# Optimization experiments

Hardware: AMD Instinct MI355X
Metric: run time of the kernel (lower is better)

Reference implementation:

```python
import jax, jax.numpy as jnp
import numpy as np

N, K, D = 131072, 256, 128


def setup_inputs() -> dict:
    key = jax.random.key(0)
    k1, k2 = jax.random.split(key, 2)
    x = jax.random.normal(k1, (N, D), dtype=jnp.float32)
    mu = jax.random.normal(k2, (K, D), dtype=jnp.float32)
    prec = jnp.ones((D,), dtype=jnp.float32)
    return {"x": x, "mu": mu, "prec": prec}


def reference(x, mu, prec):
    # measure[n,k] = -0.5 * sum_d prec[d] * (x[n,d] - mu[k,d])**2
    # Expanded quadratic form avoids materializing the (N,K,D) diff tensor:
    #   sum_d prec*(x-mu)^2 = sum_d prec*x^2 - 2*sum_d (prec*x)*mu + sum_d prec*mu^2
    x_sq = jnp.einsum('nd,d->n', x * x, prec)            # (N,)
    mu_sq = jnp.einsum('kd,d->k', mu * mu, prec)         # (K,)
    cross = jnp.einsum('nd,d,kd->nk', x, prec, mu)       # (N,K)
    m = -0.5 * (x_sq[:, None] - 2.0 * cross + mu_sq[None, :])  # (N,K)
    return -jnp.sum(jax.nn.logsumexp(m, axis=1))
```

## Files before the change

kernel.cpp:

```cpp
#include <hip/hip_runtime.h>
#include <hip/hip_bf16.h>

#define N_ROWS 131072
#define K_MIX  256
#define D_DIM  128
#define LDSB_STRIDE 136
#define B_CHUNKS (K_MIX * LDSB_STRIDE / 8)

typedef float  f32x4  __attribute__((ext_vector_type(4)));
typedef short  bf16x8 __attribute__((ext_vector_type(8)));

__device__ inline bf16x8 pack8(float4 a, float4 b) {
    union { bf16x8 v; __hip_bfloat162 h[4]; } u;
    u.h[0] = __float22bfloat162_rn(make_float2(a.x, a.y));
    u.h[1] = __float22bfloat162_rn(make_float2(a.z, a.w));
    u.h[2] = __float22bfloat162_rn(make_float2(b.x, b.y));
    u.h[3] = __float22bfloat162_rn(make_float2(b.z, b.w));
    return u.v;
}

__global__ void prep_kernel(const float* __restrict__ mu,
                            const float* __restrict__ prec,
                            unsigned short* __restrict__ Bp,
                            float* __restrict__ musq)
{
    int idx = blockIdx.x * 256 + threadIdx.x;
    int row = idx >> 5;
    int c4  = idx & 31;
    float4 mv = ((const float4*)mu)[idx];
    float4 pv = ((const float4*)prec)[c4];
    float px = mv.x * pv.x, py = mv.y * pv.y, pz = mv.z * pv.z, pw = mv.w * pv.w;
    union { ushort4 u4; __hip_bfloat162 h[2]; } h;
    h.h[0] = __float22bfloat162_rn(make_float2(px, py));
    h.h[1] = __float22bfloat162_rn(make_float2(pz, pw));
    *(ushort4*)&Bp[row * LDSB_STRIDE + c4 * 4] = h.u4;
    if (c4 == 31) {
        bf16x8 z = (bf16x8)0;
        *(bf16x8*)&Bp[row * LDSB_STRIDE + 128] = z;
    }
    float ps = px * mv.x + py * mv.y + pz * mv.z + pw * mv.w;
    ps += __shfl_xor(ps, 1);  ps += __shfl_xor(ps, 2);
    ps += __shfl_xor(ps, 4);  ps += __shfl_xor(ps, 8);
    ps += __shfl_xor(ps, 16);
    if ((threadIdx.x & 31) == 0) musq[row] = 0.5f * ps;
}

__global__ __launch_bounds__(256, 2)
void mixture_main(const float* __restrict__ x,
                  const unsigned short* __restrict__ Bp,
                  const float* __restrict__ musqg,
                  const float* __restrict__ prec,
                  float* __restrict__ out)
{
    __shared__ __align__(16) unsigned short sB[K_MIX * LDSB_STRIDE];
    __shared__ float sMusq[K_MIX];
    __shared__ float sPrec[D_DIM];
    __shared__ float sRed[4];

    const int tid  = threadIdx.x;
    const int lane = tid & 63;
    const int wave = tid >> 6;
    const int low4 = lane & 15;
    const int q    = lane >> 4;

    {
        const bf16x8* src = (const bf16x8*)Bp;
        bf16x8* dst = (bf16x8*)sB;
        #pragma unroll
        for (int i = 0; i < B_CHUNKS / 256; ++i)
            dst[i * 256 + tid] = src[i * 256 + tid];
        sMusq[tid] = -musqg[tid];
        if (tid < D_DIM) sPrec[tid] = prec[tid];
    }
    __syncthreads();

    const float4* x4 = (const float4*)x;
    const int rbase = blockIdx.x * 256 + wave * 32;
    const float4* xr0 = x4 + (size_t)(rbase + low4) * 32;
    const float4* xr1 = x4 + (size_t)(rbase + low4 + 16) * 32;

    float lacc = 0.f;

    #pragma unroll 1
    for (int rg = 0; rg < 2; ++rg) {
        const float4* p0 = xr0 + rg * 128 * 32;
        const float4* p1 = xr1 + rg * 128 * 32;

        float4 xv[4][4];
        #pragma unroll
        for (int k = 0; k < 4; ++k) {
            const int d4 = k * 8 + q * 2;
            xv[k][0] = p0[d4]; xv[k][1] = p0[d4 + 1];
            xv[k][2] = p1[d4]; xv[k][3] = p1[d4 + 1];
        }

        float xsA = 0.f, xsB = 0.f;
        bf16x8 a0[4], a1[4];
        #pragma unroll
        for (int k = 0; k < 4; ++k) {
            const int d4 = k * 8 + q * 2;
            float4 pa = *(const float4*)&sPrec[d4 * 4];
            float4 pb = *(const float4*)&sPrec[d4 * 4 + 4];
            xsA += pa.x*xv[k][0].x*xv[k][0].x + pa.y*xv[k][0].y*xv[k][0].y
                 + pa.z*xv[k][0].z*xv[k][0].z + pa.w*xv[k][0].w*xv[k][0].w;
            xsB += pb.x*xv[k][1].x*xv[k][1].x + pb.y*xv[k][1].y*xv[k][1].y
                 + pb.z*xv[k][1].z*xv[k][1].z + pb.w*xv[k][1].w*xv[k][1].w;
            xsA += pa.x*xv[k][2].x*xv[k][2].x + pa.y*xv[k][2].y*xv[k][2].y
                 + pa.z*xv[k][2].z*xv[k][2].z + pa.w*xv[k][2].w*xv[k][2].w;
            xsB += pb.x*xv[k][3].x*xv[k][3].x + pb.y*xv[k][3].y*xv[k][3].y
                 + pb.z*xv[k][3].z*xv[k][3].z + pb.w*xv[k][3].w*xv[k][3].w;
            a0[k] = pack8(xv[k][0], xv[k][1]);
            a1[k] = pack8(xv[k][2], xv[k][3]);
        }

        float m_run[2][4], s_run[2][4];
        #pragma unroll
        for (int m = 0; m < 2; ++m)
            #pragma unroll
            for (int i = 0; i < 4; ++i) { m_run[m][i] = -3.0e38f; s_run[m][i] = 0.f; }

        #pragma unroll 1
        for (int h = 0; h < 2; ++h) {
            f32x4 acc[2][8];
            #pragma unroll
            for (int c = 0; c < 8; ++c) {
                float mneg = sMusq[(h * 8 + c) * 16 + low4];
                #pragma unroll
                for (int i = 0; i < 4; ++i) { acc[0][c][i] = mneg; acc[1][c][i] = mneg; }
            }

            #pragma unroll
            for (int k = 0; k < 4; ++k) {
                #pragma unroll
                for (int c = 0; c < 8; ++c) {
                    const unsigned short* bp =
                        &sB[((h * 8 + c) * 16 + low4) * LDSB_STRIDE + k * 32 + q * 8];
                    bf16x8 b = *(const bf16x8*)bp;
                    acc[0][c] = __builtin_amdgcn_mfma_f32_16x16x32_bf16(a0[k], b, acc[0][c], 0, 0, 0);
                    acc[1][c] = __builtin_amdgcn_mfma_f32_16x16x32_bf16(a1[k], b, acc[1][c], 0, 0, 0);
                }
            }

            #pragma unroll
            for (int m = 0; m < 2; ++m) {
                #pragma unroll
                for (int i = 0; i < 4; ++i) {
                    float v0 = acc[m][0][i], v1 = acc[m][1][i];
                    float v2 = acc[m][2][i], v3 = acc[m][3][i];
                    float v4 = acc[m][4][i], v5 = acc[m][5][i];
                    float v6 = acc[m][6][i], v7 = acc[m][7][i];
                    float hmax = fmaxf(fmaxf(fmaxf(v0, v1), fmaxf(v2, v3)),
                                       fmaxf(fmaxf(v4, v5), fmaxf(v6, v7)));
                    float hsum = __expf(v0 - hmax) + __expf(v1 - hmax)
                               + __expf(v2 - hmax) + __expf(v3 - hmax)
                               + __expf(v4 - hmax) + __expf(v5 - hmax)
                               + __expf(v6 - hmax) + __expf(v7 - hmax);
                    float mr = m_run[m][i];
                    float mn = fmaxf(mr, hmax);
                    s_run[m][i] = s_run[m][i] * __expf(mr - mn) + hsum * __expf(hmax - mn);
                    m_run[m][i] = mn;
                }
            }
        }

        #pragma unroll
        for (int m = 0; m < 2; ++m) {
            #pragma unroll
            for (int i = 0; i < 4; ++i) {
                float mr = m_run[m][i], sr = s_run[m][i];
                #pragma unroll
                for (int step = 1; step <= 8; step <<= 1) {
                    float mo = __shfl_xor(mr, step);
                    float so = __shfl_xor(sr, step);
                    float mn = fmaxf(mr, mo);
                    sr = sr * __expf(mr - mn) + so * __expf(mo - mn);
                    mr = mn;
                }
                if (low4 == 0) lacc -= mr + __logf(sr);
            }
        }
        lacc += 0.5f * (xsA + xsB);
    }

    lacc += __shfl_xor(lacc, 32); lacc += __shfl_xor(lacc, 16);
    lacc += __shfl_xor(lacc, 8);  lacc += __shfl_xor(lacc, 4);
    lacc += __shfl_xor(lacc, 2);  lacc += __shfl_xor(lacc, 1);
    if (lane == 0) sRed[wave] = lacc;
    __syncthreads();
    if (tid == 0) atomicAdd(out, sRed[0] + sRed[1] + sRed[2] + sRed[3]);
}

extern "C" void kernel_launch(void* const* d_in, const int* in_sizes, int n_in,
                              void* d_out, int out_size, void* d_ws, size_t ws_size,
                              hipStream_t stream) {
    const float* x    = (const float*)d_in[0];
    const float* mu   = (const float*)d_in[1];
    const float* prec = (const float*)d_in[2];
    float* out = (float*)d_out;

    unsigned short* Bp = (unsigned short*)d_ws;
    float* musq = (float*)((char*)d_ws + K_MIX * LDSB_STRIDE * 2);

    hipMemsetAsync(d_out, 0, sizeof(float), stream);
    prep_kernel<<<32, 256, 0, stream>>>(mu, prec, Bp, musq);
    mixture_main<<<N_ROWS / 256, 256, 0, stream>>>(x, Bp, musq, prec, out);
}
```

Baseline: 112.0 us.

## Fuse mu preprocessing into main kernel, prefetch x, and use base-2 exp/log

Drops the separate prep kernel. Each block now scales mu by prec and converts it to bf16 directly into LDS, which removes one launch and the workspace round trip. The first x tile is issued before that LDS fill so its latency overlaps the setup, and the second tile is loaded before the first compute phase. prec is pre-scaled by log2(e) so the hardware exp2 and log2 builtins can replace exp and log, with a final ln2 rescale. The cost is that every one of the 512 blocks redoes the mu conversion (256x128 floats read from global or L2), and the bf16 rounding now applies to log2e-scaled values.

```diff
diff --git a/kernel.cpp b/kernel.cpp
--- a/kernel.cpp
+++ b/kernel.cpp
@@ -5,10 +5,23 @@
 #define K_MIX  256
 #define D_DIM  128
 #define LDSB_STRIDE 136
-#define B_CHUNKS (K_MIX * LDSB_STRIDE / 8)
 
 typedef float  f32x4  __attribute__((ext_vector_type(4)));
 typedef short  bf16x8 __attribute__((ext_vector_type(8)));
+
+#define LOG2E_F 1.44269504088896340736f
+#define LN2_F   0.69314718055994530942f
+
+#if __has_builtin(__builtin_amdgcn_exp2f)
+#define EXP2F(x) __builtin_amdgcn_exp2f(x)
+#else
+#define EXP2F(x) exp2f(x)
+#endif
+#if __has_builtin(__builtin_amdgcn_logf)
+#define LOG2F(x) __builtin_amdgcn_logf(x)
+#else
+#define LOG2F(x) __log2f(x)
+#endif
 
 __device__ inline bf16x8 pack8(float4 a, float4 b) {
     union { bf16x8 v; __hip_bfloat162 h[4]; } u;
@@ -19,38 +32,11 @@
     return u.v;
 }
 
-__global__ void prep_kernel(const float* __restrict__ mu,
-                            const float* __restrict__ prec,
-                            unsigned short* __restrict__ Bp,
-                            float* __restrict__ musq)
-{
-    int idx = blockIdx.x * 256 + threadIdx.x;
-    int row = idx >> 5;
-    int c4  = idx & 31;
-    float4 mv = ((const float4*)mu)[idx];
-    float4 pv = ((const float4*)prec)[c4];
-    float px = mv.x * pv.x, py = mv.y * pv.y, pz = mv.z * pv.z, pw = mv.w * pv.w;
-    union { ushort4 u4; __hip_bfloat162 h[2]; } h;
-    h.h[0] = __float22bfloat162_rn(make_float2(px, py));
-    h.h[1] = __float22bfloat162_rn(make_float2(pz, pw));
-    *(ushort4*)&Bp[row * LDSB_STRIDE + c4 * 4] = h.u4;
-    if (c4 == 31) {
-        bf16x8 z = (bf16x8)0;
-        *(bf16x8*)&Bp[row * LDSB_STRIDE + 128] = z;
-    }
-    float ps = px * mv.x + py * mv.y + pz * mv.z + pw * mv.w;
-    ps += __shfl_xor(ps, 1);  ps += __shfl_xor(ps, 2);
-    ps += __shfl_xor(ps, 4);  ps += __shfl_xor(ps, 8);
-    ps += __shfl_xor(ps, 16);
-    if ((threadIdx.x & 31) == 0) musq[row] = 0.5f * ps;
-}
-
 __global__ __launch_bounds__(256, 2)
-void mixture_main(const float* __restrict__ x,
-                  const unsigned short* __restrict__ Bp,
-                  const float* __restrict__ musqg,
-                  const float* __restrict__ prec,
-                  float* __restrict__ out)
+void mixture_fused(const float* __restrict__ x,
+                   const float* __restrict__ mu,
+                   const float* __restrict__ prec,
+                   float* __restrict__ out)
 {
     __shared__ __align__(16) unsigned short sB[K_MIX * LDSB_STRIDE];
     __shared__ float sMusq[K_MIX];
@@ -63,56 +49,72 @@
     const int low4 = lane & 15;
     const int q    = lane >> 4;
 
-    {
-        const bf16x8* src = (const bf16x8*)Bp;
-        bf16x8* dst = (bf16x8*)sB;
-        #pragma unroll
-        for (int i = 0; i < B_CHUNKS / 256; ++i)
-            dst[i * 256 + tid] = src[i * 256 + tid];
-        sMusq[tid] = -musqg[tid];
-        if (tid < D_DIM) sPrec[tid] = prec[tid];
-    }
-    __syncthreads();
-
     const float4* x4 = (const float4*)x;
     const int rbase = blockIdx.x * 256 + wave * 32;
     const float4* xr0 = x4 + (size_t)(rbase + low4) * 32;
     const float4* xr1 = x4 + (size_t)(rbase + low4 + 16) * 32;
 
+    float4 xv[4][4];
+    #pragma unroll
+    for (int k = 0; k < 4; ++k) {
+        const int d4 = k * 8 + q * 2;
+        xv[k][0] = xr0[d4]; xv[k][1] = xr0[d4 + 1];
+        xv[k][2] = xr1[d4]; xv[k][3] = xr1[d4 + 1];
+    }
+
+    if (tid < 32) {
+        float4 pv = ((const float4*)prec)[tid];
+        pv.x *= LOG2E_F; pv.y *= LOG2E_F; pv.z *= LOG2E_F; pv.w *= LOG2E_F;
+        *(float4*)&sPrec[tid * 4] = pv;
+    }
+    __syncthreads();
+
+    #pragma unroll 4
+    for (int i = 0; i < 32; ++i) {
+        const int idx = i * 256 + tid;
+        const int row = idx >> 5;
+        const int c4  = idx & 31;
+        float4 mv = ((const float4*)mu)[idx];
+        float4 pv = *(const float4*)&sPrec[c4 * 4];
+        float px = mv.x * pv.x, py = mv.y * pv.y, pz = mv.z * pv.z, pw = mv.w * pv.w;
+        union { ushort4 u4; __hip_bfloat162 h[2]; } hh;
+        hh.h[0] = __float22bfloat162_rn(make_float2(px, py));
+        hh.h[1] = __float22bfloat162_rn(make_float2(pz, pw));
+        *(ushort4*)&sB[row * LDSB_STRIDE + c4 * 4] = hh.u4;
+        float ps = px * mv.x + py * mv.y + pz * mv.z + pw * mv.w;
+        ps += __shfl_xor(ps, 1);  ps += __shfl_xor(ps, 2);
+        ps += __shfl_xor(ps, 4);  ps += __shfl_xor(ps, 8);
+        ps += __shfl_xor(ps, 16);
+        if ((tid & 31) == 0) sMusq[row] = -0.5f * ps;
+    }
+    __syncthreads();
+
     float lacc = 0.f;
-
-    #pragma unroll 1
-    for (int rg = 0; rg < 2; ++rg) {
-        const float4* p0 = xr0 + rg * 128 * 32;
-        const float4* p1 = xr1 + rg * 128 * 32;
-
-        float4 xv[4][4];
-        #pragma unroll
-        for (int k = 0; k < 4; ++k) {
-            const int d4 = k * 8 + q * 2;
-            xv[k][0] = p0[d4]; xv[k][1] = p0[d4 + 1];
-            xv[k][2] = p1[d4]; xv[k][3] = p1[d4 + 1];
-        }
-
+    bf16x8 a0[4], a1[4];
+    float xs;
+
+    auto phase2 = [&](const float4 (&v)[4][4]) {
         float xsA = 0.f, xsB = 0.f;
-        bf16x8 a0[4], a1[4];
         #pragma unroll
         for (int k = 0; k < 4; ++k) {
             const int d4 = k * 8 + q * 2;
             float4 pa = *(const float4*)&sPrec[d4 * 4];
             float4 pb = *(const float4*)&sPrec[d4 * 4 + 4];
-            xsA += pa.x*xv[k][0].x*xv[k][0].x + pa.y*xv[k][0].y*xv[k][0].y
-                 + pa.z*xv[k][0].z*xv[k][0].z + pa.w*xv[k][0].w*xv[k][0].w;
-            xsB += pb.x*xv[k][1].x*xv[k][1].x + pb.y*xv[k][1].y*xv[k][1].y
-                 + pb.z*xv[k][1].z*xv[k][1].z + pb.w*xv[k][1].w*xv[k][1].w;
-            xsA += pa.x*xv[k][2].x*xv[k][2].x + pa.y*xv[k][2].y*xv[k][2].y
-                 + pa.z*xv[k][2].z*xv[k][2].z + pa.w*xv[k][2].w*xv[k][2].w;
-            xsB += pb.x*xv[k][3].x*xv[k][3].x + pb.y*xv[k][3].y*xv[k][3].y
-                 + pb.z*xv[k][3].z*xv[k][3].z + pb.w*xv[k][3].w*xv[k][3].w;
-            a0[k] = pack8(xv[k][0], xv[k][1]);
-            a1[k] = pack8(xv[k][2], xv[k][3]);
-        }
-
+            xsA += pa.x*v[k][0].x*v[k][0].x + pa.y*v[k][0].y*v[k][0].y
+                 + pa.z*v[k][0].z*v[k][0].z + pa.w*v[k][0].w*v[k][0].w;
+            xsB += pb.x*v[k][1].x*v[k][1].x + pb.y*v[k][1].y*v[k][1].y
+                 + pb.z*v[k][1].z*v[k][1].z + pb.w*v[k][1].w*v[k][1].w;
+            xsA += pa.x*v[k][2].x*v[k][2].x + pa.y*v[k][2].y*v[k][2].y
+                 + pa.z*v[k][2].z*v[k][2].z + pa.w*v[k][2].w*v[k][2].w;
+            xsB += pb.x*v[k][3].x*v[k][3].x + pb.y*v[k][3].y*v[k][3].y
+                 + pb.z*v[k][3].z*v[k][3].z + pb.w*v[k][3].w*v[k][3].w;
+            a0[k] = pack8(v[k][0], v[k][1]);
+            a1[k] = pack8(v[k][2], v[k][3]);
+        }
+        xs = xsA + xsB;
+    };
+
+    auto compute = [&]() {
         float m_run[2][4], s_run[2][4];
         #pragma unroll
         for (int m = 0; m < 2; ++m)
@@ -151,13 +153,13 @@
                     float v6 = acc[m][6][i], v7 = acc[m][7][i];
                     float hmax = fmaxf(fmaxf(fmaxf(v0, v1), fmaxf(v2, v3)),
                                        fmaxf(fmaxf(v4, v5), fmaxf(v6, v7)));
-                    float hsum = __expf(v0 - hmax) + __expf(v1 - hmax)
-                               + __expf(v2 - hmax) + __expf(v3 - hmax)
-                               + __expf(v4 - hmax) + __expf(v5 - hmax)
-                               + __expf(v6 - hmax) + __expf(v7 - hmax);
+                    float hsum = EXP2F(v0 - hmax) + EXP2F(v1 - hmax)
+                               + EXP2F(v2 - hmax) + EXP2F(v3 - hmax)
+                               + EXP2F(v4 - hmax) + EXP2F(v5 - hmax)
+                               + EXP2F(v6 - hmax) + EXP2F(v7 - hmax);
                     float mr = m_run[m][i];
                     float mn = fmaxf(mr, hmax);
-                    s_run[m][i] = s_run[m][i] * __expf(mr - mn) + hsum * __expf(hmax - mn);
+                    s_run[m][i] = s_run[m][i] * EXP2F(mr - mn) + hsum * EXP2F(hmax - mn);
                     m_run[m][i] = mn;
                 }
             }
@@ -173,14 +175,32 @@
                     float mo = __shfl_xor(mr, step);
                     float so = __shfl_xor(sr, step);
                     float mn = fmaxf(mr, mo);
-                    sr = sr * __expf(mr - mn) + so * __expf(mo - mn);
+                    sr = sr * EXP2F(mr - mn) + so * EXP2F(mo - mn);
                     mr = mn;
                 }
-                if (low4 == 0) lacc -= mr + __logf(sr);
-            }
-        }
-        lacc += 0.5f * (xsA + xsB);
-    }
+                if (low4 == 0) lacc -= mr + LOG2F(sr);
+            }
+        }
+        lacc += 0.5f * xs;
+    };
+
+    phase2(xv);
+    {
+        const float4* p0 = xr0 + 128 * 32;
+        const float4* p1 = xr1 + 128 * 32;
+        #pragma unroll
+        for (int k = 0; k < 4; ++k) {
+            const int d4 = k * 8 + q * 2;
+            xv[k][0] = p0[d4]; xv[k][1] = p0[d4 + 1];
+            xv[k][2] = p1[d4]; xv[k][3] = p1[d4 + 1];
+        }
+    }
+    compute();
+
+    phase2(xv);
+    compute();
+
+    lacc *= LN2_F;
 
     lacc += __shfl_xor(lacc, 32); lacc += __shfl_xor(lacc, 16);
     lacc += __shfl_xor(lacc, 8);  lacc += __shfl_xor(lacc, 4);
@@ -198,10 +218,6 @@
     const float* prec = (const float*)d_in[2];
     float* out = (float*)d_out;
 
-    unsigned short* Bp = (unsigned short*)d_ws;
-    float* musq = (float*)((char*)d_ws + K_MIX * LDSB_STRIDE * 2);
-
     hipMemsetAsync(d_out, 0, sizeof(float), stream);
-    prep_kernel<<<32, 256, 0, stream>>>(mu, prec, Bp, musq);
-    mixture_main<<<N_ROWS / 256, 256, 0, stream>>>(x, Bp, musq, prec, out);
+    mixture_fused<<<N_ROWS / 256, 256, 0, stream>>>(x, mu, prec, out);
 }
```

Result: slower. 152.4 us (+36.1%).
